# Performance work log

Hardware: AMD Instinct MI355X
Metric: run time of the kernel (lower is better)

Reference implementation:

```python
import jax, jax.numpy as jnp
import numpy as np

ALPHA = 3.0      # tanhalpha
K = 10           # subgraph_size (overridden to 10 in __init__)
PROP_ALPHA = 0.05
DEPTH = 2        # gcn_depth
NUM_FEAT = 2


def _build_graph(emb1, emb2, w1, b1, w2, b2):
    # MTGNN graph_constructor: directed adjacency + row-wise top-k sparsification
    n1 = jnp.tanh(ALPHA * (emb1 @ w1 + b1))
    n2 = jnp.tanh(ALPHA * (emb2 @ w2 + b2))
    a = n1 @ n2.T - n2 @ n1.T
    adj = jax.nn.relu(jnp.tanh(ALPHA * a))          # [N, N]
    _, idx = jax.lax.top_k(adj, K)                  # keep top-K per row
    N = adj.shape[0]
    mask = jnp.zeros_like(adj).at[jnp.arange(N)[:, None], idx].set(1.0)
    return adj * mask


def _norm_adj(adj):
    a = adj + jnp.eye(adj.shape[0], dtype=adj.dtype)
    return a / a.sum(axis=1, keepdims=True)


def _mixprop(x, a_norm, w, b):
    # x: [B, C, N, L]; multi-hop diffusion then 1x1 conv over stacked hops
    h = x
    outs = [x]
    for _ in range(DEPTH):
        h = PROP_ALPHA * x + (1.0 - PROP_ALPHA) * jnp.einsum('bcwl,vw->bcvl', h, a_norm)
        outs.append(h)
    ho = jnp.concatenate(outs, axis=1)              # [B, (D+1)C, N, L]
    return jnp.einsum('bcnl,oc->bonl', ho, w) + b[None, :, None, None]


def _conv1x1(x, w, b):
    # 1x1 Conv2d over channel dim of [B, C, N, L]
    return jnp.einsum('bcnl,oc->bonl', x, w) + b[None, :, None, None]


def _forward(history_data, node_emb_u, T_i_D_emb, D_i_W_emb,
             gc_emb1, gc_emb2, gc_w1, gc_b1, gc_w2, gc_b2,
             W_emb, b_emb, Wg1, bg1, Wg2, bg2, Wsc, bsc,
             mix1_w, mix1_b, mix2_w, mix2_b,
             Wtf1, btf1, Wtf2, btf2, Wec1, bec1, Wec2, bec2,
             Wfc1, bfc1, Wfc2, bfc2, Wec3, bec3):
    # --- prepare inputs ---
    tid_idx = (history_data[..., NUM_FEAT] * 288.0).astype(jnp.int32)   # [B,T,N]
    diw_idx = history_data[..., NUM_FEAT + 1].astype(jnp.int32)
    tid = T_i_D_emb[tid_idx]                                            # [B,T,N,TE]
    diw = D_i_W_emb[diw_idx]                                            # [B,T,N,TE]
    hd = history_data[..., :NUM_FEAT]                                   # [B,T,N,F]

    adj = _build_graph(gc_emb1, gc_emb2, gc_w1, gc_b1, gc_w2, gc_b2)    # [N,N]

    hd = hd @ W_emb + b_emb                                             # [B,T,N,H]
    B, T, N, H = hd.shape

    # --- decouple gate 1 ---
    nu = jnp.broadcast_to(node_emb_u[None, None], (B, T, N, node_emb_u.shape[-1]))
    g_in = jnp.concatenate([nu, tid, diw], axis=-1)                     # [B,T,N,64]
    gate = jax.nn.sigmoid(jax.nn.relu(g_in @ Wg1 + bg1) @ Wg2 + bg2)    # [B,T,N,H]
    x1 = gate * hd
    x2 = hd - x1
    gated = jnp.concatenate([x1, x2], axis=-1)                          # [B,T,N,2H]

    # start conv acts on the T(=12) dim as channels
    x1 = jax.nn.relu(jnp.einsum('btnh,ot->bonh', x1, Wsc) + bsc[None, :, None, None])
    x2 = jax.nn.relu(jnp.einsum('btnh,ot->bonh', x2, Wsc) + bsc[None, :, None, None])

    aN = _norm_adj(adj)
    aTN = _norm_adj(adj.T)
    outs = []
    for i in range(2):
        H1 = _mixprop(x1, aN, mix1_w[i], mix1_b[i]) + _mixprop(x1, aTN, mix2_w[i], mix2_b[i])
        H2 = _mixprop(x2, aN, mix1_w[i], mix1_b[i]) + _mixprop(x2, aTN, mix2_w[i], mix2_b[i])
        outs.append(H1)
        outs.append(H2)
    out = jnp.concatenate(outs, axis=-1)                                # [B,32,N,4H]

    # TFModule: 2-layer MLP on last dim (dropout = identity in eval)
    x = jax.nn.relu(out @ Wtf1 + btf1) @ Wtf2 + btf2                    # [B,32,N,4H]

    x = jax.nn.relu(_conv1x1(x, Wec1, bec1))                            # [B,128,N,4H]
    x = _conv1x1(x, Wec2, bec2)                                         # [B,12,N,4H]

    fh = jnp.concatenate([gated, x, tid, diw, hd], axis=-1)             # [B,12,N,472]
    f = jax.nn.relu(jax.nn.relu(fh) @ Wfc1 + bfc1) @ Wfc2 + bfc2        # [B,12,N,gap]
    f = _conv1x1(f, Wec3, bec3)                                         # [B,4,N,gap]
    f = jnp.transpose(f, (0, 2, 1, 3)).reshape(B, N, -1)                # [B,N,12]
    return f


def setup_inputs() -> dict:
    key = jax.random.key(0)
    ks = iter(jax.random.split(key, 48))
    def p(*shape, s=0.1):
        return (jax.random.normal(next(ks), shape, jnp.float32) * s)
    B, T, N, F_, H, ND, TE = 8, 12, 1024, 2, 64, 40, 12
    feat = jax.random.normal(next(ks), (B, T, N, F_), jnp.float32)
    tid = jax.random.uniform(next(ks), (B, T, N, 1), jnp.float32)
    diw = jax.random.randint(next(ks), (B, T, N, 1), 0, 7).astype(jnp.float32)
    history_data = jnp.concatenate([feat, tid, diw], axis=-1)
    return {
        'history_data': history_data,
        'node_emb_u': p(N, ND), 'T_i_D_emb': p(288, TE), 'D_i_W_emb': p(7, TE),
        'gc_emb1': p(N, ND), 'gc_emb2': p(N, ND),
        'gc_w1': p(ND, ND), 'gc_b1': jnp.zeros((ND,), jnp.float32),
        'gc_w2': p(ND, ND), 'gc_b2': jnp.zeros((ND,), jnp.float32),
        'W_emb': p(F_, H), 'b_emb': jnp.zeros((H,), jnp.float32),
        'Wg1': p(ND + 2 * TE, 64), 'bg1': jnp.zeros((64,), jnp.float32),
        'Wg2': p(64, H), 'bg2': jnp.zeros((H,), jnp.float32),
        'Wsc': p(32, T), 'bsc': jnp.zeros((32,), jnp.float32),
        'mix1_w': p(2, 32, 96), 'mix1_b': jnp.zeros((2, 32), jnp.float32),
        'mix2_w': p(2, 32, 96), 'mix2_b': jnp.zeros((2, 32), jnp.float32),
        'Wtf1': p(4 * H, 256, s=0.05), 'btf1': jnp.zeros((256,), jnp.float32),
        'Wtf2': p(256, 4 * H, s=0.05), 'btf2': jnp.zeros((4 * H,), jnp.float32),
        'Wec1': p(128, 32), 'bec1': jnp.zeros((128,), jnp.float32),
        'Wec2': p(12, 128), 'bec2': jnp.zeros((12,), jnp.float32),
        'Wfc1': p(472, 512, s=0.05), 'bfc1': jnp.zeros((512,), jnp.float32),
        'Wfc2': p(512, 3, s=0.05), 'bfc2': jnp.zeros((3,), jnp.float32),
        'Wec3': p(4, 12), 'bec3': jnp.zeros((4,), jnp.float32),
    }


def reference(history_data, node_emb_u, T_i_D_emb, D_i_W_emb,
              gc_emb1, gc_emb2, gc_w1, gc_b1, gc_w2, gc_b2,
              W_emb, b_emb, Wg1, bg1, Wg2, bg2, Wsc, bsc,
              mix1_w, mix1_b, mix2_w, mix2_b,
              Wtf1, btf1, Wtf2, btf2, Wec1, bec1, Wec2, bec2,
              Wfc1, bfc1, Wfc2, bfc2, Wec3, bec3):
    return _forward(history_data, node_emb_u, T_i_D_emb, D_i_W_emb,
                    gc_emb1, gc_emb2, gc_w1, gc_b1, gc_w2, gc_b2,
                    W_emb, b_emb, Wg1, bg1, Wg2, bg2, Wsc, bsc,
                    mix1_w, mix1_b, mix2_w, mix2_b,
                    Wtf1, btf1, Wtf2, btf2, Wec1, bec1, Wec2, bec2,
                    Wfc1, bfc1, Wfc2, bfc2, Wec3, bec3)
```

## Files before the change

kernel.cpp:

```cpp
#include <hip/hip_runtime.h>
#include <math.h>

constexpr int ROWS_PER_B = 12 * 1024;

constexpr size_t F_N1 = 0;
constexpr size_t F_N2 = 40960;
constexpr size_t F_ANVAL = 81920;
constexpr size_t F_ROWVAL = 93184;
constexpr size_t F_COLSUM = 103424;
constexpr size_t F_INVCS = 104448;
constexpr size_t F_ATVAL = 105472;
constexpr size_t I_ANIDX = 115712;
constexpr size_t I_ROWIDX = 126976;
constexpr size_t I_COLCNT = 137216;
constexpr size_t I_COLOFF = 138240;
constexpr size_t I_COLFILL = 139265;
constexpr size_t I_ATIDX = 140289;
constexpr size_t F_W1P = 151552;
constexpr size_t F_W2P = 184320;
constexpr size_t F_WFCP = 217088;
constexpr size_t F_WEC1P = 339968;
constexpr size_t F_WEC2P = 342016;
constexpr size_t F_WMWP = 343040;
constexpr size_t GRAPH_FLOATS = 524288;

constexpr size_t PB_GATED = (size_t)ROWS_PER_B * 128 / 2;
constexpr size_t PB_HD = (size_t)ROWS_PER_B * 64 / 2;
constexpr size_t PB_X = (size_t)32 * 1024 * 64 / 2;
constexpr size_t PB_MIX = (size_t)32 * 1024 * 256 / 2;
constexpr size_t PB_TOTAL = PB_GATED + PB_HD + 5 * PB_X + PB_MIX;

typedef __attribute__((ext_vector_type(8))) short bf16x8;
typedef __attribute__((ext_vector_type(4))) float f32x4;

__device__ __forceinline__ unsigned short f2bf(float f) {
    unsigned u = __float_as_uint(f);
    unsigned r = (u + 0x7fffu + ((u >> 16) & 1u)) >> 16;
    return (unsigned short)r;
}
__device__ __forceinline__ float bf2f(unsigned short h) {
    return __uint_as_float((unsigned)h << 16);
}
__device__ __forceinline__ void unpack8(uint4 raw, float* f) {
    f[0] = bf2f((unsigned short)(raw.x & 0xffff)); f[1] = bf2f((unsigned short)(raw.x >> 16));
    f[2] = bf2f((unsigned short)(raw.y & 0xffff)); f[3] = bf2f((unsigned short)(raw.y >> 16));
    f[4] = bf2f((unsigned short)(raw.z & 0xffff)); f[5] = bf2f((unsigned short)(raw.z >> 16));
    f[6] = bf2f((unsigned short)(raw.w & 0xffff)); f[7] = bf2f((unsigned short)(raw.w >> 16));
}
__device__ __forceinline__ uint4 pack8(const float* f) {
    uint4 r;
    r.x = f2bf(f[0]) | ((unsigned)f2bf(f[1]) << 16);
    r.y = f2bf(f[2]) | ((unsigned)f2bf(f[3]) << 16);
    r.z = f2bf(f[4]) | ((unsigned)f2bf(f[5]) << 16);
    r.w = f2bf(f[6]) | ((unsigned)f2bf(f[7]) << 16);
    return r;
}


__global__ void k_init(int* cnt, int* fill, float* csum) {
    int t = blockIdx.x * 256 + threadIdx.x;
    if (t < 1024) { cnt[t] = 0; fill[t] = 0; csum[t] = 0.f; }
}

__global__ void k_embed(const float* e1, const float* e2, const float* w1, const float* b1,
                        const float* w2, const float* b2, float* n1, float* n2) {
    int idx = blockIdx.x * 256 + threadIdx.x;
    if (idx >= 81920) return;
    int m = idx / 40960, rem = idx - m * 40960;
    int i = rem / 40, j = rem - i * 40;
    const float* e = m ? e2 : e1;
    const float* w = m ? w2 : w1;
    const float* bv = m ? b2 : b1;
    float a = bv[j];
    for (int k = 0; k < 40; k++) a += e[i * 40 + k] * w[k * 40 + j];
    (m ? n2 : n1)[i * 40 + j] = tanhf(3.0f * a);
}

__global__ __launch_bounds__(256) void k_adj(const float* n1, const float* n2,
        float* aN_val, int* aN_idx, float* row_val, int* row_idx,
        int* col_cnt, float* col_sum) {
    __shared__ float arow[1024];
    __shared__ float n1v[40], n2v[40];
    __shared__ float rv[256];
    __shared__ int ri[256];
    __shared__ float topv[10];
    __shared__ int topi[10];
    int v = blockIdx.x, t = threadIdx.x;
    if (t < 40) { n1v[t] = n1[v * 40 + t]; n2v[t] = n2[v * 40 + t]; }
    __syncthreads();
    for (int j = t; j < 1024; j += 256) {
        float d1 = 0.f, d2 = 0.f;
        for (int k = 0; k < 40; k++) {
            d1 += n1v[k] * n2[j * 40 + k];
            d2 += n2v[k] * n1[j * 40 + k];
        }
        float a = tanhf(3.0f * (d1 - d2));
        arow[j] = a > 0.f ? a : 0.f;
    }
    __syncthreads();
    for (int r = 0; r < 10; r++) {
        float bv = -1.f; int bi = 1 << 30;
        for (int j = t; j < 1024; j += 256) {
            float x = arow[j];
            if (x > bv || (x == bv && j < bi)) { bv = x; bi = j; }
        }
        rv[t] = bv; ri[t] = bi;
        __syncthreads();
        for (int s = 128; s > 0; s >>= 1) {
            if (t < s) {
                float ov = rv[t + s]; int oi = ri[t + s];
                if (ov > rv[t] || (ov == rv[t] && oi < ri[t])) { rv[t] = ov; ri[t] = oi; }
            }
            __syncthreads();
        }
        if (t == 0) { topv[r] = rv[0]; topi[r] = ri[0]; arow[ri[0]] = -1.f; }
        __syncthreads();
    }
    if (t == 0) {
        float s = 1.f;
        for (int r = 0; r < 10; r++) s += topv[r];
        float inv = 1.f / s;
        for (int r = 0; r < 10; r++) {
            aN_idx[v * 11 + r] = topi[r];
            aN_val[v * 11 + r] = topv[r] * inv;
            row_idx[v * 10 + r] = topi[r];
            row_val[v * 10 + r] = topv[r];
            atomicAdd(&col_cnt[topi[r]], 1);
            atomicAdd(&col_sum[topi[r]], topv[r]);
        }
        aN_idx[v * 11 + 10] = v;
        aN_val[v * 11 + 10] = inv;
    }
}

__global__ __launch_bounds__(1024) void k_scan(const int* cnt, int* off,
                                               const float* csum, float* inv) {
    __shared__ int tmp[1024];
    int t = threadIdx.x;
    tmp[t] = cnt[t];
    __syncthreads();
    for (int s = 1; s < 1024; s <<= 1) {
        int v = 0;
        if (t >= s) v = tmp[t - s];
        __syncthreads();
        tmp[t] += v;
        __syncthreads();
    }
    off[t + 1] = tmp[t];
    if (t == 0) off[0] = 0;
    inv[t] = 1.0f / (csum[t] + 1.0f);
}

__global__ void k_scatter(const int* row_idx, const float* row_val, const int* off,
                          int* fill, int* aT_idx, float* aT_val) {
    int e = blockIdx.x * 256 + threadIdx.x;
    if (e >= 10240) return;
    int v = e / 10;
    int j = row_idx[e];
    int pos = off[j] + atomicAdd(&fill[j], 1);
    aT_idx[pos] = v;
    aT_val[pos] = row_val[e];
}

__global__ void k_packw(const float* W, unsigned short* out) {
    int id = blockIdx.x * 256 + threadIdx.x;
    if (id >= 8192) return;
    int lane = id & 63, rest = id >> 6;
    int nb = rest & 15, kb = rest >> 4;
    int krow = kb * 32 + (lane >> 4) * 8;
    int col = nb * 16 + (lane & 15);
    unsigned short v[8];
#pragma unroll
    for (int j = 0; j < 8; j++) v[j] = f2bf(W[(size_t)(krow + j) * 256 + col]);
#pragma unroll
    for (int j = 0; j < 8; j++) out[(size_t)id * 8 + j] = v[j];
}

__global__ void k_packfc(const float* W, unsigned short* out) {
    int id = blockIdx.x * 256 + threadIdx.x;
    if (id >= 30720) return;
    int lane = id & 63, rest = id >> 6;
    int nb = rest & 31, kb = rest >> 5;
    int k0 = kb * 32 + (lane >> 4) * 8;
    int col = nb * 16 + (lane & 15);
    unsigned short v[8];
#pragma unroll
    for (int j = 0; j < 8; j++) {
        int k = k0 + j;
        v[j] = (k < 472) ? f2bf(W[(size_t)k * 512 + col]) : (unsigned short)0;
    }
#pragma unroll
    for (int j = 0; j < 8; j++) out[(size_t)id * 8 + j] = v[j];
}

__global__ void k_packec(const float* W1, const float* W2,
                         unsigned short* o1, unsigned short* o2) {
    int id = blockIdx.x * 256 + threadIdx.x;
    if (id < 512) {
        int mt = id >> 6, lane = id & 63;
        int o = mt * 16 + (lane & 15);
        int c0 = (lane >> 4) * 8;
#pragma unroll
        for (int j = 0; j < 8; j++)
            o1[(size_t)id * 8 + j] = f2bf(W1[o * 32 + c0 + j]);
    } else if (id < 768) {
        int id2 = id - 512;
        int kb = id2 >> 6, lane = id2 & 63;
        int p = lane & 15;
        int k0 = kb * 32 + (lane >> 4) * 8;
#pragma unroll
        for (int j = 0; j < 8; j++)
            o2[(size_t)id2 * 8 + j] = (p < 12) ? f2bf(W2[p * 128 + k0 + j])
                                               : (unsigned short)0;
    }
}

__global__ void k_packmw(const float* mw1, const float* mw2, unsigned short* out) {
    int id = blockIdx.x * 256 + threadIdx.x;
    if (id >= 1536) return;
    int f = id >> 6, lane = id & 63;
    int kb = f >> 2, rt = f & 3;
    int row = rt * 16 + (lane & 15);
    int ph = (kb >= 3) ? 1 : 0;
    int kloc = (kb - ph * 3) * 32 + (lane >> 4) * 8;
    const float* mw = ph ? mw2 : mw1;
#pragma unroll
    for (int j = 0; j < 8; j++)
        out[(size_t)id * 8 + j] = f2bf(mw[row * 96 + kloc + j]);
}


__global__ __launch_bounds__(256) void k_gate(const float* hist, const float* nodeu,
        const float* tide, const float* diwe,
        const float* Wg1, const float* bg1, const float* Wg2, const float* bg2,
        const float* Wemb, const float* bemb, unsigned short* gated, unsigned short* hd_emb) {
    __shared__ float w1[4096], w2[4096];
    __shared__ float gin[4][64], hid[4][64];
    __shared__ float sb1[64], sb2[64], we[128], be[64];
    int t = threadIdx.x;
    for (int i = t; i < 4096; i += 256) { w1[i] = Wg1[i]; w2[i] = Wg2[i]; }
    if (t < 64) { sb1[t] = bg1[t]; sb2[t] = bg2[t]; be[t] = bemb[t]; }
    if (t < 128) we[t] = Wemb[t];
    int r = t >> 6, lane = t & 63;
    int row = blockIdx.x * 4 + r;
    int n = row & 1023;
    const float* hrow = hist + (size_t)row * 4;
    float f0 = hrow[0], f1 = hrow[1];
    int tid_i = (int)(hrow[2] * 288.0f);
    int diw_i = (int)hrow[3];
    float g;
    if (lane < 40) g = nodeu[n * 40 + lane];
    else if (lane < 52) g = tide[tid_i * 12 + lane - 40];
    else g = diwe[diw_i * 12 + lane - 52];
    gin[r][lane] = g;
    __syncthreads();
    float acc = sb1[lane];
    for (int k = 0; k < 64; k++) acc += gin[r][k] * w1[k * 64 + lane];
    hid[r][lane] = acc > 0.f ? acc : 0.f;
    __syncthreads();
    acc = sb2[lane];
    for (int k = 0; k < 64; k++) acc += hid[r][k] * w2[k * 64 + lane];
    float gate = 1.f / (1.f + expf(-acc));
    float hd = f0 * we[lane] + f1 * we[64 + lane] + be[lane];
    float x1 = gate * hd;
    gated[(size_t)row * 128 + lane] = f2bf(x1);
    gated[(size_t)row * 128 + 64 + lane] = f2bf(hd - x1);
    hd_emb[(size_t)row * 64 + lane] = f2bf(hd);
}

__global__ __launch_bounds__(256) void k_wsc(const unsigned short* gated, const float* Wsc,
                                             const float* bsc, unsigned short* xs, int xoff) {
    __shared__ float w[384];
    __shared__ float sb[32];
    int t = threadIdx.x;
    if (t < 384) w[t] = Wsc[t];
    if (t < 32) sb[t] = bsc[t];
    __syncthreads();
    int idx = blockIdx.x * 256 + t;
    int h = idx & 63, n = (idx >> 6) & 1023, b = idx >> 16;
    float xv[12];
#pragma unroll
    for (int tt = 0; tt < 12; tt++)
        xv[tt] = bf2f(gated[(size_t)((b * 12 + tt) * 1024 + n) * 128 + xoff + h]);
#pragma unroll
    for (int o = 0; o < 32; o++) {
        float a = sb[o];
#pragma unroll
        for (int tt = 0; tt < 12; tt++) a += xv[tt] * w[o * 12 + tt];
        xs[(size_t)((b * 32 + o) * 1024 + n) * 64 + h] = f2bf(a > 0.f ? a : 0.f);
    }
}

__global__ __launch_bounds__(256) void k_spmm2(unsigned short* out1, unsigned short* out2,
        const unsigned short* x, const unsigned short* hin1, const unsigned short* hin2,
        const int* aN_idx, const float* aN_val,
        const int* aT_idx, const float* aT_val,
        const int* off, const float* inv_cs) {
    int nper = gridDim.x >> 3;
    int bid = (blockIdx.x & 7) * nper + (blockIdx.x >> 3);
    int t = threadIdx.x;
    int l8 = t & 7, r = t >> 3;
    int g = bid * 32 + r;
    int v = g & 1023, bc = g >> 10;
    size_t rowoff = (size_t)bc * 65536;
    float hv[8];
    const unsigned short* base1 = hin1 + rowoff;
    float s1[8];
#pragma unroll
    for (int j = 0; j < 8; j++) s1[j] = 0.f;
#pragma unroll
    for (int e = 0; e < 11; e++) {
        int w = aN_idx[v * 11 + e];
        float a = aN_val[v * 11 + e];
        uint4 raw = *(const uint4*)(base1 + (size_t)w * 64 + l8 * 8);
        unpack8(raw, hv);
#pragma unroll
        for (int j = 0; j < 8; j++) s1[j] += a * hv[j];
    }
    const unsigned short* base2 = hin2 + rowoff;
    float s2[8];
    {
        uint4 raw = *(const uint4*)(base2 + (size_t)v * 64 + l8 * 8);
        unpack8(raw, s2);
        int e0 = off[v], e1 = off[v + 1];
        for (int e = e0; e < e1; e++) {
            int w = aT_idx[e];
            float a = aT_val[e];
            uint4 rw = *(const uint4*)(base2 + (size_t)w * 64 + l8 * 8);
            unpack8(rw, hv);
#pragma unroll
            for (int j = 0; j < 8; j++) s2[j] += a * hv[j];
        }
        float ic = inv_cs[v];
#pragma unroll
        for (int j = 0; j < 8; j++) s2[j] *= ic;
    }
    uint4 xr = *(const uint4*)(x + (size_t)g * 64 + l8 * 8);
    float xv[8];
    unpack8(xr, xv);
    float o1[8], o2[8];
#pragma unroll
    for (int j = 0; j < 8; j++) {
        float xb = 0.05f * xv[j];
        o1[j] = xb + 0.95f * s1[j];
        o2[j] = xb + 0.95f * s2[j];
    }
    *(uint4*)(out1 + (size_t)g * 64 + l8 * 8) = pack8(o1);
    *(uint4*)(out2 + (size_t)g * 64 + l8 * 8) = pack8(o2);
}

__global__ __launch_bounds__(256) void k_proj(const unsigned short* xs,
        const unsigned short* h1, const unsigned short* h2,
        const unsigned short* h1b, const unsigned short* h2b,
        const unsigned short* mwp, const float* m1b, const float* m2b,
        unsigned short* mix, int xp) {
    __shared__ unsigned short Bf[24 * 64 * 8];
    int t = threadIdx.x;
    int wave = t >> 6, l = t & 63;
    int lr = l & 15, lg = l >> 4;
    int b = blockIdx.x >> 10, n = blockIdx.x & 1023;
#pragma unroll
    for (int i = 0; i < 6; i++) {
        int f = wave * 6 + i;
        int kb = f >> 2, nt = f & 3;
        int ph = (kb >= 3) ? 1 : 0;
        int q = kb - ph * 3;
        const unsigned short* Hq = (q == 0) ? xs : (q == 1 ? (ph ? h1b : h1)
                                                           : (ph ? h2b : h2));
        const unsigned short* src = Hq + ((size_t)(b * 32 + lg * 8) * 1024 + n) * 64
                                       + nt * 16 + lr;
        bf16x8 v;
#pragma unroll
        for (int j = 0; j < 8; j++)
            v[j] = (short)src[(size_t)j * 65536];
        *(bf16x8*)(Bf + ((size_t)f * 64 + l) * 8) = v;
    }
    __syncthreads();
    f32x4 acc[4];
#pragma unroll
    for (int nt = 0; nt < 4; nt++) {
        f32x4 c;
#pragma unroll
        for (int r = 0; r < 4; r++) {
            int row = wave * 16 + lg * 4 + r;
            c[r] = m1b[row] + m2b[row];
        }
        acc[nt] = c;
    }
#pragma unroll
    for (int kb = 0; kb < 6; kb++) {
        bf16x8 af = *(const bf16x8*)(mwp + (size_t)((kb * 4 + wave) * 64 + l) * 8);
#pragma unroll
        for (int nt = 0; nt < 4; nt++) {
            bf16x8 bfv = *(const bf16x8*)(Bf + ((size_t)(kb * 4 + nt) * 64 + l) * 8);
            acc[nt] = __builtin_amdgcn_mfma_f32_16x16x32_bf16(af, bfv, acc[nt], 0, 0, 0);
        }
    }
#pragma unroll
    for (int nt = 0; nt < 4; nt++)
#pragma unroll
        for (int r = 0; r < 4; r++) {
            int row = wave * 16 + lg * 4 + r;
            int i2 = row >> 5, o = row & 31;
            mix[(size_t)((b * 32 + o) * 1024 + n) * 256 + (i2 * 2 + xp) * 64 + nt * 16 + lr]
                = f2bf(acc[nt][r]);
        }
}

__global__ __launch_bounds__(256) void k_tf(unsigned short* mix, const unsigned short* W1p,
                                            const float* B1, const unsigned short* W2p,
                                            const float* B2) {
    __shared__ unsigned short Abuf[32 * 256];
    __shared__ unsigned short Hbuf[32 * 256];
    int t = threadIdx.x;
    int wave = t >> 6, l = t & 63;
    size_t row0 = (size_t)blockIdx.x * 32;
    const uint4* src = (const uint4*)(mix + row0 * 256);
#pragma unroll
    for (int it = 0; it < 4; it++) {
        int f = t + it * 256;
        uint4 raw = src[f];
        int e = f * 8, row = e >> 8, col = e & 255;
        int byte = (row * 512 + col * 2) ^ ((row & 7) << 4);
        *(uint4*)((char*)Abuf + byte) = raw;
    }
    __syncthreads();
    int colg0 = wave * 64;
    int lr = l & 15, lg = l >> 4;
    f32x4 acc[2][4];
#pragma unroll
    for (int nb = 0; nb < 4; nb++) {
        float bv = B1[colg0 + nb * 16 + lr];
        f32x4 c; c[0] = bv; c[1] = bv; c[2] = bv; c[3] = bv;
        acc[0][nb] = c; acc[1][nb] = c;
    }
#pragma unroll
    for (int kb = 0; kb < 8; kb++) {
        int k2 = (kb * 32 + lg * 8) * 2;
        int by0 = (lr * 512 + k2) ^ ((lr & 7) << 4);
        int by1 = ((16 + lr) * 512 + k2) ^ ((lr & 7) << 4);
        bf16x8 a0 = *(const bf16x8*)((char*)Abuf + by0);
        bf16x8 a1 = *(const bf16x8*)((char*)Abuf + by1);
#pragma unroll
        for (int nb = 0; nb < 4; nb++) {
            int nbg = wave * 4 + nb;
            bf16x8 bw = *(const bf16x8*)(W1p + (size_t)((kb * 16 + nbg) * 64 + l) * 8);
            acc[0][nb] = __builtin_amdgcn_mfma_f32_16x16x32_bf16(a0, bw, acc[0][nb], 0, 0, 0);
            acc[1][nb] = __builtin_amdgcn_mfma_f32_16x16x32_bf16(a1, bw, acc[1][nb], 0, 0, 0);
        }
    }
#pragma unroll
    for (int rb = 0; rb < 2; rb++)
#pragma unroll
        for (int nb = 0; nb < 4; nb++)
#pragma unroll
            for (int r = 0; r < 4; r++) {
                int row = rb * 16 + lg * 4 + r;
                int col = colg0 + nb * 16 + lr;
                unsigned short h = f2bf(fmaxf(acc[rb][nb][r], 0.f));
                int byte = (row * 512 + col * 2) ^ ((row & 7) << 4);
                *(unsigned short*)((char*)Hbuf + byte) = h;
            }
    __syncthreads();
#pragma unroll
    for (int nb = 0; nb < 4; nb++) {
        float bv = B2[colg0 + nb * 16 + lr];
        f32x4 c; c[0] = bv; c[1] = bv; c[2] = bv; c[3] = bv;
        acc[0][nb] = c; acc[1][nb] = c;
    }
#pragma unroll
    for (int kb = 0; kb < 8; kb++) {
        int k2 = (kb * 32 + lg * 8) * 2;
        int by0 = (lr * 512 + k2) ^ ((lr & 7) << 4);
        int by1 = ((16 + lr) * 512 + k2) ^ ((lr & 7) << 4);
        bf16x8 a0 = *(const bf16x8*)((char*)Hbuf + by0);
        bf16x8 a1 = *(const bf16x8*)((char*)Hbuf + by1);
#pragma unroll
        for (int nb = 0; nb < 4; nb++) {
            int nbg = wave * 4 + nb;
            bf16x8 bw = *(const bf16x8*)(W2p + (size_t)((kb * 16 + nbg) * 64 + l) * 8);
            acc[0][nb] = __builtin_amdgcn_mfma_f32_16x16x32_bf16(a0, bw, acc[0][nb], 0, 0, 0);
            acc[1][nb] = __builtin_amdgcn_mfma_f32_16x16x32_bf16(a1, bw, acc[1][nb], 0, 0, 0);
        }
    }
#pragma unroll
    for (int rb = 0; rb < 2; rb++)
#pragma unroll
        for (int nb = 0; nb < 4; nb++)
#pragma unroll
            for (int r = 0; r < 4; r++) {
                int row = rb * 16 + lg * 4 + r;
                int col = colg0 + nb * 16 + lr;
                mix[(row0 + row) * 256 + col] = f2bf(acc[rb][nb][r]);
            }
}

__global__ __launch_bounds__(256) void k_ec(const unsigned short* tfo,
        const unsigned short* W1p, const float* B1,
        const unsigned short* W2p, const float* B2, unsigned short* eco) {
    __shared__ unsigned short Hl[4 * 64 * 48];
    int t = threadIdx.x;
    int wave = t >> 6, l = t & 63;
    int lr = l & 15, lg = l >> 4;
    int b = blockIdx.x >> 10, n = blockIdx.x & 1023;
    int lbase = wave * 64;
    unsigned short* myH = Hl + wave * 3072;
    const unsigned short* xb = tfo + ((size_t)(b * 32) * 1024 + n) * 256;
    bf16x8 xf[4];
#pragma unroll
    for (int nt = 0; nt < 4; nt++) {
        int ll = lbase + nt * 16 + lr;
        bf16x8 v;
#pragma unroll
        for (int j = 0; j < 8; j++)
            v[j] = (short)xb[(size_t)(lg * 8 + j) * 262144 + ll];
        xf[nt] = v;
    }
    f32x4 d2[4];
    {
        f32x4 c;
#pragma unroll
        for (int r = 0; r < 4; r++) {
            int p = lg * 4 + r;
            c[r] = (p < 12) ? B2[p] : 0.f;
        }
#pragma unroll
        for (int nt = 0; nt < 4; nt++) d2[nt] = c;
    }
#pragma unroll
    for (int ch = 0; ch < 4; ch++) {
        f32x4 h[2][4];
#pragma unroll
        for (int mt = 0; mt < 2; mt++) {
            f32x4 c;
#pragma unroll
            for (int r = 0; r < 4; r++) c[r] = B1[ch * 32 + mt * 16 + lg * 4 + r];
#pragma unroll
            for (int nt = 0; nt < 4; nt++) h[mt][nt] = c;
        }
#pragma unroll
        for (int mt = 0; mt < 2; mt++) {
            bf16x8 aw = *(const bf16x8*)(W1p + (size_t)((ch * 2 + mt) * 64 + l) * 8);
#pragma unroll
            for (int nt = 0; nt < 4; nt++)
                h[mt][nt] = __builtin_amdgcn_mfma_f32_16x16x32_bf16(aw, xf[nt], h[mt][nt], 0, 0, 0);
        }
#pragma unroll
        for (int mt = 0; mt < 2; mt++)
#pragma unroll
            for (int nt = 0; nt < 4; nt++) {
                unsigned lo = f2bf(fmaxf(h[mt][nt][0], 0.f)) |
                              ((unsigned)f2bf(fmaxf(h[mt][nt][1], 0.f)) << 16);
                unsigned hi = f2bf(fmaxf(h[mt][nt][2], 0.f)) |
                              ((unsigned)f2bf(fmaxf(h[mt][nt][3], 0.f)) << 16);
                uint2 pk; pk.x = lo; pk.y = hi;
                *(uint2*)(myH + (nt * 16 + lr) * 48 + mt * 16 + lg * 4) = pk;
            }
        bf16x8 aw2 = *(const bf16x8*)(W2p + (size_t)(ch * 64 + l) * 8);
#pragma unroll
        for (int nt = 0; nt < 4; nt++) {
            bf16x8 hf = *(const bf16x8*)(myH + (nt * 16 + lr) * 48 + lg * 8);
            d2[nt] = __builtin_amdgcn_mfma_f32_16x16x32_bf16(aw2, hf, d2[nt], 0, 0, 0);
        }
    }
#pragma unroll
    for (int nt = 0; nt < 4; nt++)
#pragma unroll
        for (int r = 0; r < 4; r++) {
            int p = lg * 4 + r;
            if (p < 12) {
                int ll = lbase + nt * 16 + lr;
                eco[((size_t)(b * 12 + p) * 1024 + n) * 256 + ll] = f2bf(d2[nt][r]);
            }
        }
}

__global__ __launch_bounds__(256) void k_fc(const unsigned short* gated, const unsigned short* eco,
        const unsigned short* hd_emb, const float* hist, const float* tide, const float* diwe,
        const unsigned short* W1p, const float* B1, const float* W2, const float* B2,
        float* fbuf) {
    __shared__ unsigned short Abuf[16 * 480];
    __shared__ unsigned short Hbuf[16 * 512];
    int t = threadIdx.x;
    int wave = t >> 6, l = t & 63;
    int lr = l & 15, lg = l >> 4;
    int row0 = blockIdx.x * 16;
#pragma unroll
    for (int it = 0; it < 8; it++) {
        int idx = it * 256 + t;
        if (idx < 1920) {
            int row = idx / 120;
            int col = (idx - row * 120) * 4;
            int grow = row0 + row;
            int n = grow & 1023, bt = grow >> 10;
            int b = bt / 12, tt = bt - b * 12;
            unsigned short w[4];
            if (col < 128) {
                uint2 raw = *(const uint2*)&gated[(size_t)grow * 128 + col];
                w[0] = raw.x & 0xffff; w[1] = raw.x >> 16;
                w[2] = raw.y & 0xffff; w[3] = raw.y >> 16;
            } else if (col < 384) {
                uint2 raw = *(const uint2*)&eco[(size_t)((b * 12 + tt) * 1024 + n) * 256 + (col - 128)];
                w[0] = raw.x & 0xffff; w[1] = raw.x >> 16;
                w[2] = raw.y & 0xffff; w[3] = raw.y >> 16;
            } else if (col < 396) {
                int tid_i = (int)(hist[(size_t)grow * 4 + 2] * 288.0f);
#pragma unroll
                for (int q = 0; q < 4; q++) w[q] = f2bf(fmaxf(tide[tid_i * 12 + col - 384 + q], 0.f));
            } else if (col < 408) {
                int diw_i = (int)hist[(size_t)grow * 4 + 3];
#pragma unroll
                for (int q = 0; q < 4; q++) w[q] = f2bf(fmaxf(diwe[diw_i * 12 + col - 396 + q], 0.f));
            } else if (col < 472) {
                uint2 raw = *(const uint2*)&hd_emb[(size_t)grow * 64 + col - 408];
                w[0] = raw.x & 0xffff; w[1] = raw.x >> 16;
                w[2] = raw.y & 0xffff; w[3] = raw.y >> 16;
            } else {
#pragma unroll
                for (int q = 0; q < 4; q++) w[q] = 0;
            }
#pragma unroll
            for (int q = 0; q < 4; q++) if (w[q] >> 15) w[q] = 0;
            uint2 pk;
            pk.x = w[0] | ((unsigned)w[1] << 16);
            pk.y = w[2] | ((unsigned)w[3] << 16);
            int byte = (row * 960 + col * 2) ^ ((row & 7) << 4);
            *(uint2*)((char*)Abuf + byte) = pk;
        }
    }
    __syncthreads();
    int colg0 = wave * 128;
    f32x4 acc[8];
#pragma unroll
    for (int nb = 0; nb < 8; nb++) {
        float bv = B1[colg0 + nb * 16 + lr];
        f32x4 c; c[0] = bv; c[1] = bv; c[2] = bv; c[3] = bv;
        acc[nb] = c;
    }
#pragma unroll
    for (int kb = 0; kb < 15; kb++) {
        int k2 = (kb * 32 + lg * 8) * 2;
        int by0 = (lr * 960 + k2) ^ ((lr & 7) << 4);
        bf16x8 a0 = *(const bf16x8*)((char*)Abuf + by0);
#pragma unroll
        for (int nb = 0; nb < 8; nb++) {
            int nbg = wave * 8 + nb;
            bf16x8 bw = *(const bf16x8*)(W1p + (size_t)((kb * 32 + nbg) * 64 + l) * 8);
            acc[nb] = __builtin_amdgcn_mfma_f32_16x16x32_bf16(a0, bw, acc[nb], 0, 0, 0);
        }
    }
#pragma unroll
    for (int nb = 0; nb < 8; nb++)
#pragma unroll
        for (int r = 0; r < 4; r++) {
            int row = lg * 4 + r;
            int col = colg0 + nb * 16 + lr;
            unsigned short h = f2bf(fmaxf(acc[nb][r], 0.f));
            int byte = (row * 1024 + col * 2) ^ ((row & 7) << 4);
            *(unsigned short*)((char*)Hbuf + byte) = h;
        }
    __syncthreads();
    float* redp = (float*)Abuf;
    {
        int rsub = t >> 5, seg = t & 31;
#pragma unroll
        for (int rg = 0; rg < 2; rg++) {
            int r = rg * 8 + rsub;
            float p0 = 0.f, p1 = 0.f, p2 = 0.f;
#pragma unroll
            for (int j = 0; j < 16; j++) {
                int k = seg + j * 32;
                int byte = (r * 1024 + k * 2) ^ ((r & 7) << 4);
                float h = bf2f(*(const unsigned short*)((char*)Hbuf + byte));
                p0 += h * W2[k * 3];
                p1 += h * W2[k * 3 + 1];
                p2 += h * W2[k * 3 + 2];
            }
            redp[r * 96 + seg] = p0;
            redp[r * 96 + 32 + seg] = p1;
            redp[r * 96 + 64 + seg] = p2;
        }
    }
    __syncthreads();
    if (t < 48) {
        int rr = t / 3, p = t - rr * 3;
        float s = B2[p];
        for (int seg = 0; seg < 32; seg++) s += redp[rr * 96 + p * 32 + seg];
        fbuf[(size_t)(row0 + rr) * 3 + p] = s;
    }
}

__global__ void k_ec3(const float* f, const float* W, const float* bv, float* out) {
    int idx = blockIdx.x * 256 + threadIdx.x;
    int l = idx % 3;
    int rest = idx / 3;
    int o = rest & 3;
    int n = (rest >> 2) & 1023;
    int b = rest >> 12;
    float s = bv[o];
#pragma unroll
    for (int c = 0; c < 12; c++)
        s += f[(size_t)((b * 12 + c) * 1024 + n) * 3 + l] * W[o * 12 + c];
    out[idx] = s;
}

extern "C" void kernel_launch(void* const* d_in, const int* in_sizes, int n_in,
                              void* d_out, int out_size, void* d_ws, size_t ws_size,
                              hipStream_t stream) {
    const float* hist = (const float*)d_in[0];
    const float* node_emb_u = (const float*)d_in[1];
    const float* T_i_D_emb = (const float*)d_in[2];
    const float* D_i_W_emb = (const float*)d_in[3];
    const float* gc_emb1 = (const float*)d_in[4];
    const float* gc_emb2 = (const float*)d_in[5];
    const float* gc_w1 = (const float*)d_in[6];
    const float* gc_b1 = (const float*)d_in[7];
    const float* gc_w2 = (const float*)d_in[8];
    const float* gc_b2 = (const float*)d_in[9];
    const float* W_emb = (const float*)d_in[10];
    const float* b_emb = (const float*)d_in[11];
    const float* Wg1 = (const float*)d_in[12];
    const float* bg1 = (const float*)d_in[13];
    const float* Wg2 = (const float*)d_in[14];
    const float* bg2 = (const float*)d_in[15];
    const float* Wsc = (const float*)d_in[16];
    const float* bsc = (const float*)d_in[17];
    const float* mix1_w = (const float*)d_in[18];
    const float* mix1_b = (const float*)d_in[19];
    const float* mix2_w = (const float*)d_in[20];
    const float* mix2_b = (const float*)d_in[21];
    const float* Wtf1 = (const float*)d_in[22];
    const float* btf1 = (const float*)d_in[23];
    const float* Wtf2 = (const float*)d_in[24];
    const float* btf2 = (const float*)d_in[25];
    const float* Wec1 = (const float*)d_in[26];
    const float* bec1 = (const float*)d_in[27];
    const float* Wec2 = (const float*)d_in[28];
    const float* bec2 = (const float*)d_in[29];
    const float* Wfc1 = (const float*)d_in[30];
    const float* bfc1 = (const float*)d_in[31];
    const float* Wfc2 = (const float*)d_in[32];
    const float* bfc2 = (const float*)d_in[33];
    const float* Wec3 = (const float*)d_in[34];
    const float* bec3 = (const float*)d_in[35];

    float* ws = (float*)d_ws;
    float* n1 = ws + F_N1;
    float* n2 = ws + F_N2;
    float* aN_val = ws + F_ANVAL;
    float* row_val = ws + F_ROWVAL;
    float* col_sum = ws + F_COLSUM;
    float* inv_cs = ws + F_INVCS;
    float* aT_val = ws + F_ATVAL;
    int* aN_idx = (int*)(ws + I_ANIDX);
    int* row_idx = (int*)(ws + I_ROWIDX);
    int* col_cnt = (int*)(ws + I_COLCNT);
    int* col_off = (int*)(ws + I_COLOFF);
    int* col_fill = (int*)(ws + I_COLFILL);
    int* aT_idx = (int*)(ws + I_ATIDX);
    unsigned short* w1p = (unsigned short*)(ws + F_W1P);
    unsigned short* w2p = (unsigned short*)(ws + F_W2P);
    unsigned short* wfcp = (unsigned short*)(ws + F_WFCP);
    unsigned short* wec1p = (unsigned short*)(ws + F_WEC1P);
    unsigned short* wec2p = (unsigned short*)(ws + F_WEC2P);
    unsigned short* wmwp = (unsigned short*)(ws + F_WMWP);

    size_t avail = ws_size / 4;
    int CB = 8;
    while (CB > 1 && GRAPH_FLOATS + (size_t)CB * PB_TOTAL > avail) CB >>= 1;
    int nchunk = 8 / CB;

    unsigned short* gated = (unsigned short*)(ws + GRAPH_FLOATS);
    unsigned short* hd_emb = (unsigned short*)(ws + GRAPH_FLOATS + (size_t)CB * PB_GATED);
    unsigned short* xs = (unsigned short*)(ws + GRAPH_FLOATS + (size_t)CB * (PB_GATED + PB_HD));
    unsigned short* h1 = xs + (size_t)CB * PB_X * 2;
    unsigned short* h2 = h1 + (size_t)CB * PB_X * 2;
    unsigned short* h1b = h2 + (size_t)CB * PB_X * 2;
    unsigned short* h2b = h1b + (size_t)CB * PB_X * 2;
    unsigned short* mix = h2b + (size_t)CB * PB_X * 2;
    unsigned short* eco = xs;
    float* fbuf = (float*)h2b;

    k_init<<<4, 256, 0, stream>>>(col_cnt, col_fill, col_sum);
    k_embed<<<320, 256, 0, stream>>>(gc_emb1, gc_emb2, gc_w1, gc_b1, gc_w2, gc_b2, n1, n2);
    k_adj<<<1024, 256, 0, stream>>>(n1, n2, aN_val, aN_idx, row_val, row_idx, col_cnt, col_sum);
    k_scan<<<1, 1024, 0, stream>>>(col_cnt, col_off, col_sum, inv_cs);
    k_scatter<<<40, 256, 0, stream>>>(row_idx, row_val, col_off, col_fill, aT_idx, aT_val);
    k_packw<<<32, 256, 0, stream>>>(Wtf1, w1p);
    k_packw<<<32, 256, 0, stream>>>(Wtf2, w2p);
    k_packfc<<<120, 256, 0, stream>>>(Wfc1, wfcp);
    k_packec<<<3, 256, 0, stream>>>(Wec1, Wec2, wec1p, wec2p);
    k_packmw<<<6, 256, 0, stream>>>(mix1_w, mix2_w, wmwp);

    for (int ch = 0; ch < nchunk; ch++) {
        const float* hist_c = hist + (size_t)ch * CB * ROWS_PER_B * 4;
        float* out_c = (float*)d_out + (size_t)ch * CB * ROWS_PER_B;

        k_gate<<<CB * 3072, 256, 0, stream>>>(hist_c, node_emb_u, T_i_D_emb, D_i_W_emb,
                                              Wg1, bg1, Wg2, bg2, W_emb, b_emb, gated, hd_emb);
        for (int xp = 0; xp < 2; xp++) {
            k_wsc<<<CB * 256, 256, 0, stream>>>(gated, Wsc, bsc, xs, xp * 64);
            k_spmm2<<<CB * 1024, 256, 0, stream>>>(h1, h1b, xs, xs, xs,
                                                   aN_idx, aN_val, aT_idx, aT_val,
                                                   col_off, inv_cs);
            k_spmm2<<<CB * 1024, 256, 0, stream>>>(h2, h2b, xs, h1, h1b,
                                                   aN_idx, aN_val, aT_idx, aT_val,
                                                   col_off, inv_cs);
            k_proj<<<CB * 1024, 256, 0, stream>>>(xs, h1, h2, h1b, h2b,
                                                  wmwp, mix1_b, mix2_b, mix, xp);
        }
        k_tf<<<CB * 1024, 256, 0, stream>>>(mix, w1p, btf1, w2p, btf2);
        k_ec<<<CB * 1024, 256, 0, stream>>>(mix, wec1p, bec1, wec2p, bec2, eco);
        k_fc<<<CB * 768, 256, 0, stream>>>(gated, eco, hd_emb, hist_c, T_i_D_emb, D_i_W_emb,
                                           wfcp, bfc1, Wfc2, bfc2, fbuf);
        k_ec3<<<CB * 48, 256, 0, stream>>>(fbuf, Wec3, bec3, out_c);
    }
}
```

Baseline: 1.247 ms.

## Load FC1 A-fragments directly from global and reduce FC2 in registers

```diff
diff --git a/kernel.cpp b/kernel.cpp
--- a/kernel.cpp
+++ b/kernel.cpp
@@ -54,6 +54,14 @@
     r.z = f2bf(f[4]) | ((unsigned)f2bf(f[5]) << 16);
     r.w = f2bf(f[6]) | ((unsigned)f2bf(f[7]) << 16);
     return r;
+}
+__device__ __forceinline__ bf16x8 relu8(bf16x8 v) {
+#pragma unroll
+    for (int j = 0; j < 8; j++) {
+        unsigned short u = (unsigned short)v[j];
+        v[j] = (short)((u >> 15) ? 0 : u);
+    }
+    return v;
 }
 
 
@@ -577,58 +585,20 @@
 
 __global__ __launch_bounds__(256) void k_fc(const unsigned short* gated, const unsigned short* eco,
         const unsigned short* hd_emb, const float* hist, const float* tide, const float* diwe,
-        const unsigned short* W1p, const float* B1, const float* W2, const float* B2,
-        float* fbuf) {
-    __shared__ unsigned short Abuf[16 * 480];
-    __shared__ unsigned short Hbuf[16 * 512];
+        const unsigned short* W1p, const float* B1, const float* W2,
+        float* pbuf) {
     int t = threadIdx.x;
     int wave = t >> 6, l = t & 63;
     int lr = l & 15, lg = l >> 4;
     int row0 = blockIdx.x * 16;
-#pragma unroll
-    for (int it = 0; it < 8; it++) {
-        int idx = it * 256 + t;
-        if (idx < 1920) {
-            int row = idx / 120;
-            int col = (idx - row * 120) * 4;
-            int grow = row0 + row;
-            int n = grow & 1023, bt = grow >> 10;
-            int b = bt / 12, tt = bt - b * 12;
-            unsigned short w[4];
-            if (col < 128) {
-                uint2 raw = *(const uint2*)&gated[(size_t)grow * 128 + col];
-                w[0] = raw.x & 0xffff; w[1] = raw.x >> 16;
-                w[2] = raw.y & 0xffff; w[3] = raw.y >> 16;
-            } else if (col < 384) {
-                uint2 raw = *(const uint2*)&eco[(size_t)((b * 12 + tt) * 1024 + n) * 256 + (col - 128)];
-                w[0] = raw.x & 0xffff; w[1] = raw.x >> 16;
-                w[2] = raw.y & 0xffff; w[3] = raw.y >> 16;
-            } else if (col < 396) {
-                int tid_i = (int)(hist[(size_t)grow * 4 + 2] * 288.0f);
-#pragma unroll
-                for (int q = 0; q < 4; q++) w[q] = f2bf(fmaxf(tide[tid_i * 12 + col - 384 + q], 0.f));
-            } else if (col < 408) {
-                int diw_i = (int)hist[(size_t)grow * 4 + 3];
-#pragma unroll
-                for (int q = 0; q < 4; q++) w[q] = f2bf(fmaxf(diwe[diw_i * 12 + col - 396 + q], 0.f));
-            } else if (col < 472) {
-                uint2 raw = *(const uint2*)&hd_emb[(size_t)grow * 64 + col - 408];
-                w[0] = raw.x & 0xffff; w[1] = raw.x >> 16;
-                w[2] = raw.y & 0xffff; w[3] = raw.y >> 16;
-            } else {
-#pragma unroll
-                for (int q = 0; q < 4; q++) w[q] = 0;
-            }
-#pragma unroll
-            for (int q = 0; q < 4; q++) if (w[q] >> 15) w[q] = 0;
-            uint2 pk;
-            pk.x = w[0] | ((unsigned)w[1] << 16);
-            pk.y = w[2] | ((unsigned)w[3] << 16);
-            int byte = (row * 960 + col * 2) ^ ((row & 7) << 4);
-            *(uint2*)((char*)Abuf + byte) = pk;
-        }
-    }
-    __syncthreads();
+    int grow = row0 + lr;
+    int n = grow & 1023, bt = grow >> 10;
+    int b = bt / 12, tt = bt - b * 12;
+    const unsigned short* gptr = gated + (size_t)grow * 128;
+    const unsigned short* eptr = eco + (size_t)((b * 12 + tt) * 1024 + n) * 256;
+    const unsigned short* hptr = hd_emb + (size_t)grow * 64;
+    int tid_i = (int)(hist[(size_t)grow * 4 + 2] * 288.0f);
+    int diw_i = (int)hist[(size_t)grow * 4 + 3];
     int colg0 = wave * 128;
     f32x4 acc[8];
 #pragma unroll
@@ -639,58 +609,71 @@
     }
 #pragma unroll
     for (int kb = 0; kb < 15; kb++) {
-        int k2 = (kb * 32 + lg * 8) * 2;
-        int by0 = (lr * 960 + k2) ^ ((lr & 7) << 4);
-        bf16x8 a0 = *(const bf16x8*)((char*)Abuf + by0);
+        int off = kb * 32 + lg * 8;
+        bf16x8 af;
+        if (kb <= 3) {
+            af = relu8(*(const bf16x8*)(gptr + off));
+        } else if (kb <= 11) {
+            af = relu8(*(const bf16x8*)(eptr + off - 128));
+        } else if (kb == 12) {
+#pragma unroll
+            for (int j = 0; j < 8; j++) {
+                int k = off + j;
+                float v;
+                if (k < 396) v = tide[tid_i * 12 + k - 384];
+                else if (k < 408) v = diwe[diw_i * 12 + k - 396];
+                else v = bf2f(hptr[k - 408]);
+                af[j] = (short)f2bf(fmaxf(v, 0.f));
+            }
+        } else if (kb == 13) {
+            af = relu8(*(const bf16x8*)(hptr + off - 408));
+        } else {
+            if (lg < 3) af = relu8(*(const bf16x8*)(hptr + off - 408));
+            else {
+#pragma unroll
+                for (int j = 0; j < 8; j++) af[j] = 0;
+            }
+        }
 #pragma unroll
         for (int nb = 0; nb < 8; nb++) {
-            int nbg = wave * 8 + nb;
-            bf16x8 bw = *(const bf16x8*)(W1p + (size_t)((kb * 32 + nbg) * 64 + l) * 8);
-            acc[nb] = __builtin_amdgcn_mfma_f32_16x16x32_bf16(a0, bw, acc[nb], 0, 0, 0);
-        }
-    }
-#pragma unroll
-    for (int nb = 0; nb < 8; nb++)
+            bf16x8 bw = *(const bf16x8*)(W1p + (size_t)((kb * 32 + wave * 8 + nb) * 64 + l) * 8);
+            acc[nb] = __builtin_amdgcn_mfma_f32_16x16x32_bf16(af, bw, acc[nb], 0, 0, 0);
+        }
+    }
+    float p[4][3];
+#pragma unroll
+    for (int r = 0; r < 4; r++) { p[r][0] = 0.f; p[r][1] = 0.f; p[r][2] = 0.f; }
+#pragma unroll
+    for (int nb = 0; nb < 8; nb++) {
+        int col = colg0 + nb * 16 + lr;
+        float w0 = W2[col * 3], w1 = W2[col * 3 + 1], w2 = W2[col * 3 + 2];
 #pragma unroll
         for (int r = 0; r < 4; r++) {
-            int row = lg * 4 + r;
-            int col = colg0 + nb * 16 + lr;
-            unsigned short h = f2bf(fmaxf(acc[nb][r], 0.f));
-            int byte = (row * 1024 + col * 2) ^ ((row & 7) << 4);
-            *(unsigned short*)((char*)Hbuf + byte) = h;
-        }
-    __syncthreads();
-    float* redp = (float*)Abuf;
-    {
-        int rsub = t >> 5, seg = t & 31;
-#pragma unroll
-        for (int rg = 0; rg < 2; rg++) {
-            int r = rg * 8 + rsub;
-            float p0 = 0.f, p1 = 0.f, p2 = 0.f;
-#pragma unroll
-            for (int j = 0; j < 16; j++) {
-                int k = seg + j * 32;
-                int byte = (r * 1024 + k * 2) ^ ((r & 7) << 4);
-                float h = bf2f(*(const unsigned short*)((char*)Hbuf + byte));
-                p0 += h * W2[k * 3];
-                p1 += h * W2[k * 3 + 1];
-                p2 += h * W2[k * 3 + 2];
-            }
-            redp[r * 96 + seg] = p0;
-            redp[r * 96 + 32 + seg] = p1;
-            redp[r * 96 + 64 + seg] = p2;
-        }
-    }
-    __syncthreads();
-    if (t < 48) {
-        int rr = t / 3, p = t - rr * 3;
-        float s = B2[p];
-        for (int seg = 0; seg < 32; seg++) s += redp[rr * 96 + p * 32 + seg];
-        fbuf[(size_t)(row0 + rr) * 3 + p] = s;
-    }
-}
-
-__global__ void k_ec3(const float* f, const float* W, const float* bv, float* out) {
+            float h = fmaxf(acc[nb][r], 0.f);
+            p[r][0] += h * w0; p[r][1] += h * w1; p[r][2] += h * w2;
+        }
+    }
+#pragma unroll
+    for (int off = 8; off >= 1; off >>= 1)
+#pragma unroll
+        for (int r = 0; r < 4; r++) {
+            p[r][0] += __shfl_xor(p[r][0], off);
+            p[r][1] += __shfl_xor(p[r][1], off);
+            p[r][2] += __shfl_xor(p[r][2], off);
+        }
+    if (lr == 0) {
+#pragma unroll
+        for (int r = 0; r < 4; r++) {
+            size_t gr = (size_t)(row0 + lg * 4 + r);
+#pragma unroll
+            for (int pp = 0; pp < 3; pp++)
+                pbuf[gr * 12 + wave * 3 + pp] = p[r][pp];
+        }
+    }
+}
+
+__global__ void k_ec3(const float* pbuf, const float* B2, const float* W, const float* bv,
+                      float* out) {
     int idx = blockIdx.x * 256 + threadIdx.x;
     int l = idx % 3;
     int rest = idx / 3;
@@ -699,8 +682,11 @@
     int b = rest >> 12;
     float s = bv[o];
 #pragma unroll
-    for (int c = 0; c < 12; c++)
-        s += f[(size_t)((b * 12 + c) * 1024 + n) * 3 + l] * W[o * 12 + c];
+    for (int c = 0; c < 12; c++) {
+        const float* pb = pbuf + ((size_t)(b * 12 + c) * 1024 + n) * 12;
+        float fv = B2[l] + pb[l] + pb[3 + l] + pb[6 + l] + pb[9 + l];
+        s += fv * W[o * 12 + c];
+    }
     out[idx] = s;
 }
 
@@ -812,7 +798,7 @@
         k_tf<<<CB * 1024, 256, 0, stream>>>(mix, w1p, btf1, w2p, btf2);
         k_ec<<<CB * 1024, 256, 0, stream>>>(mix, wec1p, bec1, wec2p, bec2, eco);
         k_fc<<<CB * 768, 256, 0, stream>>>(gated, eco, hd_emb, hist_c, T_i_D_emb, D_i_W_emb,
-                                           wfcp, bfc1, Wfc2, bfc2, fbuf);
-        k_ec3<<<CB * 48, 256, 0, stream>>>(fbuf, Wec3, bec3, out_c);
-    }
-}
+                                           wfcp, bfc1, Wfc2, fbuf);
+        k_ec3<<<CB * 48, 256, 0, stream>>>(fbuf, bfc2, Wec3, bec3, out_c);
+    }
+}
```

Measured after the change: 1.187 ms. -4.9%, faster.
